# Performance work log

Measured on AMD Instinct MI355X. Metric: run time of the kernel, lower is better.

## Reference

```python
import jax, jax.numpy as jnp
import numpy as np

DIM = 256
HEADS = 8
DIM_HEAD = 32
INNER = HEADS * DIM_HEAD  # 256
SCALE = DIM_HEAD ** -0.5


def setup_inputs() -> dict:
    key = jax.random.key(0)
    k1, k2, k3, k4, k5, k6 = jax.random.split(key, 6)
    b, n, m = 2, 8192, 32
    x = jax.random.normal(k1, (b, n, DIM), dtype=jnp.float32)
    y = jax.random.normal(k2, (b, n, m, DIM), dtype=jnp.float32)
    # torch nn.Linear weights: [out, in]; store as [in, out] for x @ W
    s = 1.0 / np.sqrt(DIM)
    Wq = jax.random.uniform(k3, (DIM, INNER), jnp.float32, -s, s)
    Wkv = jax.random.uniform(k4, (DIM, 2 * INNER), jnp.float32, -s, s)
    so = 1.0 / np.sqrt(INNER)
    Wout = jax.random.uniform(k5, (INNER, DIM), jnp.float32, -so, so)
    bout = jax.random.uniform(k6, (DIM,), jnp.float32, -so, so)
    return {"x": x, "y": y, "Wq": Wq, "Wkv": Wkv, "Wout": Wout, "bout": bout}


def reference(x, y, Wq, Wkv, Wout, bout):
    b, n, m, _ = y.shape
    q = (x @ Wq).reshape(b, n, HEADS, DIM_HEAD)              # [b,n,h,d]
    kv = y @ Wkv                                              # [b,n,m,2*inner]
    k, v = jnp.split(kv, 2, axis=-1)
    k = k.reshape(b, n, m, HEADS, DIM_HEAD)                   # [b,n,m,h,d]
    v = v.reshape(b, n, m, HEADS, DIM_HEAD)
    dots = jnp.einsum('bnhd,bnmhd->bnhm', q, k) * SCALE       # per-token q_len=1 attention
    attn = jax.nn.softmax(dots, axis=-1)
    out = jnp.einsum('bnhm,bnmhd->bnhd', attn, v)
    out = out.reshape(b, n, INNER)
    return out @ Wout + bout
```

## Files before the change

kernel.cpp:

```cpp
#include <hip/hip_runtime.h>
#include <hip/hip_bf16.h>
#include <stdint.h>


typedef unsigned short u16;
typedef __attribute__((ext_vector_type(8))) short bf16x8;
typedef __attribute__((ext_vector_type(4))) float f32x4;
typedef __attribute__((ext_vector_type(4))) unsigned int u32x4;

#define NTOK 16384
#define SCALE_F 0.17677669529663687f

__device__ __forceinline__ u16 f2b(float v) {
  union { __hip_bfloat16 b; u16 s; } u;
  u.b = __float2bfloat16(v);
  return u.s;
}

__device__ __forceinline__ bf16x8 cvt8(f32x4 a, f32x4 b) {
  union { bf16x8 v; __hip_bfloat162 h[4]; } u;
  u.h[0] = __float22bfloat162_rn(float2{a[0], a[1]});
  u.h[1] = __float22bfloat162_rn(float2{a[2], a[3]});
  u.h[2] = __float22bfloat162_rn(float2{b[0], b[1]});
  u.h[3] = __float22bfloat162_rn(float2{b[2], b[3]});
  return u.v;
}

__device__ __forceinline__ void gll16(const float* g, const float* l) {
  __builtin_amdgcn_global_load_lds((const __attribute__((address_space(1))) void*)g,
                                   (__attribute__((address_space(3))) void*)l,
                                   16, 0, 0);
}

__global__ __launch_bounds__(256) void k0a(const float* __restrict__ Wq,
                                           const float* __restrict__ Wkv,
                                           u16* __restrict__ WqkT) {
  __shared__ float wq[16][260];
  __shared__ float wk[16][260];
  int tid = threadIdx.x;
  int e0 = blockIdx.x * 16, c0 = blockIdx.y * 16;
  {
    int r = tid >> 4, cs = (tid & 15) * 16;
#pragma unroll
    for (int i = 0; i < 4; i++) {
      *(f32x4*)&wq[r][cs + i * 4] = *(const f32x4*)(Wq + (e0 + r) * 256 + cs + i * 4);
      *(f32x4*)&wk[r][cs + i * 4] = *(const f32x4*)(Wkv + (c0 + r) * 512 + cs + i * 4);
    }
  }
  __syncthreads();
  int e = tid & 15, c = tid >> 4;
#pragma unroll
  for (int h = 0; h < 8; h++) {
    float acc = 0.f;
#pragma unroll
    for (int d = 0; d < 32; d++) acc += wq[e][h * 32 + d] * wk[c][h * 32 + d];
    WqkT[(h * 256 + c0 + c) * 256 + e0 + e] = f2b(acc * SCALE_F);
  }
}

__global__ __launch_bounds__(256) void k0b(const float* __restrict__ Wkv,
                                           const float* __restrict__ Wout,
                                           u16* __restrict__ WvoT) {
  __shared__ float wv[16][260];
  __shared__ float wo[256][20];
  int tid = threadIdx.x;
  int o0 = blockIdx.x * 16, c0 = blockIdx.y * 16;
  {
    int r = tid >> 4, cs = (tid & 15) * 16;
#pragma unroll
    for (int i = 0; i < 4; i++)
      *(f32x4*)&wv[r][cs + i * 4] = *(const f32x4*)(Wkv + (c0 + r) * 512 + 256 + cs + i * 4);
#pragma unroll
    for (int i = 0; i < 4; i++)
      *(f32x4*)&wo[tid][i * 4] = *(const f32x4*)(Wout + tid * 256 + o0 + i * 4);
  }
  __syncthreads();
  int o = tid >> 4, c = tid & 15;
  union { u16 s[8]; u32x4 v; } pk;
#pragma unroll
  for (int h = 0; h < 8; h++) {
    float acc = 0.f;
#pragma unroll
    for (int d = 0; d < 32; d++) acc += wv[c][h * 32 + d] * wo[h * 32 + d][o];
    pk.s[h] = f2b(acc);
  }
  *(u32x4*)(WvoT + (o0 + o) * 2048 + (c0 + c) * 8) = pk.v;
}

__global__ __launch_bounds__(256) void k1(const float* __restrict__ X,
                                          const u16* __restrict__ WqkT,
                                          u16* __restrict__ qW) {
  __shared__ u16 As[128][72];
  __shared__ u16 Bs[128][72];
  int tid = threadIdx.x;
  int wave = tid >> 6, lane = tid & 63;
  int l15 = lane & 15, kg = lane >> 4;
  int m0 = blockIdx.x * 128, n0 = blockIdx.y * 128;
  int sr = tid >> 1, sk = (tid & 1) * 32;
  f32x4 acc[4][4] = {};
  for (int kc = 0; kc < 256; kc += 64) {
#pragma unroll
    for (int i = 0; i < 4; i++) {
      f32x4 a = *(const f32x4*)(X + (size_t)(m0 + sr) * 256 + kc + sk + i * 8);
      f32x4 b = *(const f32x4*)(X + (size_t)(m0 + sr) * 256 + kc + sk + i * 8 + 4);
      *(bf16x8*)&As[sr][sk + i * 8] = cvt8(a, b);
      *(u32x4*)&Bs[sr][sk + i * 8] = *(const u32x4*)(WqkT + (n0 + sr) * 256 + kc + sk + i * 8);
    }
    __syncthreads();
    int rb = (wave >> 1) * 64, cb = (wave & 1) * 64;
#pragma unroll
    for (int ks = 0; ks < 2; ks++) {
      bf16x8 af[4], bfm[4];
#pragma unroll
      for (int i = 0; i < 4; i++) af[i] = *(const bf16x8*)&As[rb + i * 16 + l15][ks * 32 + kg * 8];
#pragma unroll
      for (int i = 0; i < 4; i++) bfm[i] = *(const bf16x8*)&Bs[cb + i * 16 + l15][ks * 32 + kg * 8];
#pragma unroll
      for (int mt = 0; mt < 4; mt++)
#pragma unroll
        for (int nt = 0; nt < 4; nt++)
          acc[mt][nt] = __builtin_amdgcn_mfma_f32_16x16x32_bf16(af[mt], bfm[nt], acc[mt][nt], 0, 0, 0);
    }
    __syncthreads();
  }
  int rb = m0 + (wave >> 1) * 64, cb = n0 + (wave & 1) * 64;
  int q = lane >> 4;
#pragma unroll
  for (int mt = 0; mt < 4; mt++)
#pragma unroll
    for (int nt = 0; nt < 4; nt++)
#pragma unroll
      for (int r = 0; r < 4; r++)
        qW[(size_t)(rb + mt * 16 + q * 4 + r) * 2048 + cb + nt * 16 + l15] = f2b(acc[mt][nt][r]);
}

__global__ __launch_bounds__(256) void k2(const float* __restrict__ Y,
                                          const u16* __restrict__ qW,
                                          u16* __restrict__ ybar) {
  __shared__ float ybuf[2][32][256];
  int tid = threadIdx.x;
  int wave = tid >> 6, lane = tid & 63;
  int l15 = lane & 15, kg = lane >> 4;
  int h8 = l15 & 7;
  int t0 = blockIdx.x * 32;

  {
    const float* g = Y + (size_t)t0 * 8192;
#pragma unroll
    for (int r = 0; r < 8; r++) {
      int row = wave * 8 + r;
      gll16(g + row * 256 + ((lane ^ (row & 7)) << 2), &ybuf[0][row][0]);
    }
  }
  __syncthreads();

#pragma unroll 1
  for (int i = 0; i < 32; i++) {
    int t = t0 + i;
    if (i + 1 < 32) {
      const float* g = Y + (size_t)(t + 1) * 8192;
      int b = (i + 1) & 1;
#pragma unroll
      for (int r = 0; r < 8; r++) {
        int row = wave * 8 + r;
        gll16(g + row * 256 + ((lane ^ (row & 7)) << 2), &ybuf[b][row][0]);
      }
    }
    const float (*buf)[256] = ybuf[i & 1];

    f32x4 D[2] = {f32x4{0.f, 0.f, 0.f, 0.f}, f32x4{0.f, 0.f, 0.f, 0.f}};
    const u16* qwt = qW + ((size_t)t << 11) + h8 * 256 + kg * 8;
    bf16x8 bfr[8];
#pragma unroll
    for (int s = 0; s < 8; s++) bfr[s] = *(const bf16x8*)(qwt + s * 32);
#pragma unroll
    for (int s = 0; s < 8; s++) {
#pragma unroll
      for (int mt = 0; mt < 2; mt++) {
        int row = mt * 16 + l15;
        int g0 = s * 8 + kg * 2;
        f32x4 y0 = *(const f32x4*)&buf[row][((g0) ^ (row & 7)) << 2];
        f32x4 y1 = *(const f32x4*)&buf[row][((g0 + 1) ^ (row & 7)) << 2];
        D[mt] = __builtin_amdgcn_mfma_f32_16x16x32_bf16(cvt8(y0, y1), bfr[s], D[mt], 0, 0, 0);
      }
    }

    float mx = -1e30f;
#pragma unroll
    for (int mt = 0; mt < 2; mt++)
#pragma unroll
      for (int r = 0; r < 4; r++) mx = fmaxf(mx, D[mt][r]);
    mx = fmaxf(mx, __shfl_xor(mx, 16));
    mx = fmaxf(mx, __shfl_xor(mx, 32));
    float sum = 0.f;
    float at[2][4];
#pragma unroll
    for (int mt = 0; mt < 2; mt++)
#pragma unroll
      for (int r = 0; r < 4; r++) {
        float e = __expf(D[mt][r] - mx);
        at[mt][r] = e;
        sum += e;
      }
    sum += __shfl_xor(sum, 16);
    sum += __shfl_xor(sum, 32);
    float inv = 1.0f / sum;
#pragma unroll
    for (int mt = 0; mt < 2; mt++)
#pragma unroll
      for (int r = 0; r < 4; r++) at[mt][r] *= inv;

    float acc0[4] = {0.f, 0.f, 0.f, 0.f};
    float acc1[4] = {0.f, 0.f, 0.f, 0.f};
#pragma unroll
    for (int mi = 0; mi < 8; mi++) {
      int mt = mi >> 2, q = mi & 3;
      float a0[4], a1[4];
#pragma unroll
      for (int r = 0; r < 4; r++) {
        a0[r] = __shfl(at[mt][r], q * 16 + wave * 2);
        a1[r] = __shfl(at[mt][r], q * 16 + wave * 2 + 1);
      }
#pragma unroll
      for (int r = 0; r < 4; r++) {
        int m = mt * 16 + q * 4 + r;
        f32x4 yv = *(const f32x4*)&buf[m][(lane ^ (m & 7)) << 2];
        acc0[0] += a0[r] * yv[0];
        acc0[1] += a0[r] * yv[1];
        acc0[2] += a0[r] * yv[2];
        acc0[3] += a0[r] * yv[3];
        acc1[0] += a1[r] * yv[0];
        acc1[1] += a1[r] * yv[1];
        acc1[2] += a1[r] * yv[2];
        acc1[3] += a1[r] * yv[3];
      }
    }
    u16* op = ybar + ((size_t)t << 11) + lane * 32 + wave * 2;
#pragma unroll
    for (int ci = 0; ci < 4; ci++) {
      __hip_bfloat162 pr = __float22bfloat162_rn(float2{acc0[ci], acc1[ci]});
      *(__hip_bfloat162*)(op + ci * 8) = pr;
    }
    __syncthreads();
  }
}

__global__ __launch_bounds__(256) void k3(const u16* __restrict__ Yb,
                                          const u16* __restrict__ WvoT,
                                          const float* __restrict__ bout,
                                          float* __restrict__ Out) {
  __shared__ u16 As[128][72];
  __shared__ u16 Bs[128][72];
  int tid = threadIdx.x;
  int wave = tid >> 6, lane = tid & 63;
  int l15 = lane & 15, kg = lane >> 4;
  int m0 = blockIdx.x * 128, n0 = blockIdx.y * 128;
  int sr = tid >> 1, sk = (tid & 1) * 32;
  f32x4 acc[4][4] = {};
#pragma unroll 1
  for (int kc = 0; kc < 2048; kc += 64) {
#pragma unroll
    for (int i = 0; i < 4; i++) {
      *(u32x4*)&As[sr][sk + i * 8] = *(const u32x4*)(Yb + (size_t)(m0 + sr) * 2048 + kc + sk + i * 8);
      *(u32x4*)&Bs[sr][sk + i * 8] = *(const u32x4*)(WvoT + (size_t)(n0 + sr) * 2048 + kc + sk + i * 8);
    }
    __syncthreads();
    int rb = (wave >> 1) * 64, cb = (wave & 1) * 64;
#pragma unroll
    for (int ks = 0; ks < 2; ks++) {
      bf16x8 af[4], bfm[4];
#pragma unroll
      for (int i = 0; i < 4; i++) af[i] = *(const bf16x8*)&As[rb + i * 16 + l15][ks * 32 + kg * 8];
#pragma unroll
      for (int i = 0; i < 4; i++) bfm[i] = *(const bf16x8*)&Bs[cb + i * 16 + l15][ks * 32 + kg * 8];
#pragma unroll
      for (int mt = 0; mt < 4; mt++)
#pragma unroll
        for (int nt = 0; nt < 4; nt++)
          acc[mt][nt] = __builtin_amdgcn_mfma_f32_16x16x32_bf16(af[mt], bfm[nt], acc[mt][nt], 0, 0, 0);
    }
    __syncthreads();
  }
  int rb = m0 + (wave >> 1) * 64, cb = n0 + (wave & 1) * 64;
  int q = lane >> 4;
#pragma unroll
  for (int nt = 0; nt < 4; nt++) {
    float bv = bout[cb + nt * 16 + l15];
#pragma unroll
    for (int mt = 0; mt < 4; mt++)
#pragma unroll
      for (int r = 0; r < 4; r++)
        Out[(size_t)(rb + mt * 16 + q * 4 + r) * 256 + cb + nt * 16 + l15] = acc[mt][nt][r] + bv;
  }
}

extern "C" void kernel_launch(void* const* d_in, const int* in_sizes, int n_in,
                              void* d_out, int out_size, void* d_ws, size_t ws_size,
                              hipStream_t stream) {
  const float* x    = (const float*)d_in[0];
  const float* y    = (const float*)d_in[1];
  const float* Wq   = (const float*)d_in[2];
  const float* Wkv  = (const float*)d_in[3];
  const float* Wout = (const float*)d_in[4];
  const float* bout = (const float*)d_in[5];
  float* out = (float*)d_out;

  char* ws = (char*)d_ws;
  u16* qW   = (u16*)(ws);
  u16* ybar = (u16*)(ws + ((size_t)64 << 20));
  u16* WqkT = (u16*)(ws + ((size_t)128 << 20));
  u16* WvoT = (u16*)(ws + ((size_t)129 << 20));

  k0a<<<dim3(16, 16), 256, 0, stream>>>(Wq, Wkv, WqkT);
  k0b<<<dim3(16, 16), 256, 0, stream>>>(Wkv, Wout, WvoT);
  k1<<<dim3(128, 16), 256, 0, stream>>>(x, WqkT, qW);
  k2<<<dim3(512), 256, 0, stream>>>(y, qW, ybar);
  k3<<<dim3(128, 2), 256, 0, stream>>>(ybar, WvoT, bout, out);
}
```

Baseline: 858.4 us.

## Restructure attention kernel to single-wave blocks with register-prefetched qW

The y-streaming attention kernel goes from 4-wave blocks covering 32 tokens each to 1-wave blocks covering 16 tokens each, launched as 1024 blocks. Each wave now computes all 8 heads per token, with attention weights passed through shared memory instead of cross-lane shuffles. The double-buffered LDS is replaced by one buffer refilled after the compute, guarded by explicit waitcnt, and the next token's qW fragments are prefetched into registers. The aims are to drop block-wide barriers, raise occupancy and widen the output stores, at the cost of less latency hiding for the y loads, since the wave stalls on vmcnt(0) each iteration.

Result: faster. 839.6 us (-2.2%).

```diff
diff --git a/kernel.cpp b/kernel.cpp
--- a/kernel.cpp
+++ b/kernel.cpp
@@ -134,45 +134,35 @@
         qW[(size_t)(rb + mt * 16 + q * 4 + r) * 2048 + cb + nt * 16 + l15] = f2b(acc[mt][nt][r]);
 }
 
-__global__ __launch_bounds__(256) void k2(const float* __restrict__ Y,
-                                          const u16* __restrict__ qW,
-                                          u16* __restrict__ ybar) {
-  __shared__ float ybuf[2][32][256];
-  int tid = threadIdx.x;
-  int wave = tid >> 6, lane = tid & 63;
+__global__ __launch_bounds__(64) void k2(const float* __restrict__ Y,
+                                         const u16* __restrict__ qW,
+                                         u16* __restrict__ ybar) {
+  __shared__ float buf[32][256];
+  __shared__ float attn_s[32][8];
+  int lane = threadIdx.x;
   int l15 = lane & 15, kg = lane >> 4;
   int h8 = l15 & 7;
-  int t0 = blockIdx.x * 32;
+  int t0 = blockIdx.x * 16;
 
   {
     const float* g = Y + (size_t)t0 * 8192;
 #pragma unroll
-    for (int r = 0; r < 8; r++) {
-      int row = wave * 8 + r;
-      gll16(g + row * 256 + ((lane ^ (row & 7)) << 2), &ybuf[0][row][0]);
-    }
-  }
-  __syncthreads();
+    for (int r = 0; r < 32; r++)
+      gll16(g + r * 256 + ((lane ^ (r & 7)) << 2), &buf[r][0]);
+  }
+  bf16x8 bfr[8];
+  {
+    const u16* qwt = qW + ((size_t)t0 << 11) + h8 * 256 + kg * 8;
+#pragma unroll
+    for (int s = 0; s < 8; s++) bfr[s] = *(const bf16x8*)(qwt + s * 32);
+  }
 
 #pragma unroll 1
-  for (int i = 0; i < 32; i++) {
+  for (int i = 0; i < 16; i++) {
     int t = t0 + i;
-    if (i + 1 < 32) {
-      const float* g = Y + (size_t)(t + 1) * 8192;
-      int b = (i + 1) & 1;
-#pragma unroll
-      for (int r = 0; r < 8; r++) {
-        int row = wave * 8 + r;
-        gll16(g + row * 256 + ((lane ^ (row & 7)) << 2), &ybuf[b][row][0]);
-      }
-    }
-    const float (*buf)[256] = ybuf[i & 1];
+    asm volatile("s_waitcnt vmcnt(0)" ::: "memory");
 
     f32x4 D[2] = {f32x4{0.f, 0.f, 0.f, 0.f}, f32x4{0.f, 0.f, 0.f, 0.f}};
-    const u16* qwt = qW + ((size_t)t << 11) + h8 * 256 + kg * 8;
-    bf16x8 bfr[8];
-#pragma unroll
-    for (int s = 0; s < 8; s++) bfr[s] = *(const bf16x8*)(qwt + s * 32);
 #pragma unroll
     for (int s = 0; s < 8; s++) {
 #pragma unroll
@@ -183,6 +173,12 @@
         f32x4 y1 = *(const f32x4*)&buf[row][((g0 + 1) ^ (row & 7)) << 2];
         D[mt] = __builtin_amdgcn_mfma_f32_16x16x32_bf16(cvt8(y0, y1), bfr[s], D[mt], 0, 0, 0);
       }
+    }
+
+    if (i + 1 < 16) {
+      const u16* qn = qW + ((size_t)(t + 1) << 11) + h8 * 256 + kg * 8;
+#pragma unroll
+      for (int s = 0; s < 8; s++) bfr[s] = *(const bf16x8*)(qn + s * 32);
     }
 
     float mx = -1e30f;
@@ -210,38 +206,49 @@
 #pragma unroll
       for (int r = 0; r < 4; r++) at[mt][r] *= inv;
 
-    float acc0[4] = {0.f, 0.f, 0.f, 0.f};
-    float acc1[4] = {0.f, 0.f, 0.f, 0.f};
-#pragma unroll
-    for (int mi = 0; mi < 8; mi++) {
-      int mt = mi >> 2, q = mi & 3;
-      float a0[4], a1[4];
-#pragma unroll
-      for (int r = 0; r < 4; r++) {
-        a0[r] = __shfl(at[mt][r], q * 16 + wave * 2);
-        a1[r] = __shfl(at[mt][r], q * 16 + wave * 2 + 1);
+    if (l15 < 8) {
+#pragma unroll
+      for (int mt = 0; mt < 2; mt++)
+#pragma unroll
+        for (int r = 0; r < 4; r++)
+          attn_s[mt * 16 + kg * 4 + r][l15] = at[mt][r];
+    }
+
+    float acc[8][4] = {};
+#pragma unroll
+    for (int m = 0; m < 32; m++) {
+      f32x4 yv = *(const f32x4*)&buf[m][(lane ^ (m & 7)) << 2];
+      f32x4 a0 = *(const f32x4*)&attn_s[m][0];
+      f32x4 a1 = *(const f32x4*)&attn_s[m][4];
+#pragma unroll
+      for (int h = 0; h < 4; h++)
+#pragma unroll
+        for (int c = 0; c < 4; c++) {
+          acc[h][c]     += a0[h] * yv[c];
+          acc[h + 4][c] += a1[h] * yv[c];
+        }
+    }
+
+    asm volatile("s_waitcnt lgkmcnt(0)" ::: "memory");
+
+    if (i + 1 < 16) {
+      const float* g = Y + (size_t)(t + 1) * 8192;
+#pragma unroll
+      for (int r = 0; r < 32; r++)
+        gll16(g + r * 256 + ((lane ^ (r & 7)) << 2), &buf[r][0]);
+    }
+
+    u16* op = ybar + ((size_t)t << 11) + lane * 32;
+#pragma unroll
+    for (int ci = 0; ci < 4; ci++) {
+      union { u16 s[8]; u32x4 v; } pk;
+#pragma unroll
+      for (int j = 0; j < 4; j++) {
+        __hip_bfloat162 pr = __float22bfloat162_rn(float2{acc[2 * j][ci], acc[2 * j + 1][ci]});
+        *(__hip_bfloat162*)&pk.s[2 * j] = pr;
       }
-#pragma unroll
-      for (int r = 0; r < 4; r++) {
-        int m = mt * 16 + q * 4 + r;
-        f32x4 yv = *(const f32x4*)&buf[m][(lane ^ (m & 7)) << 2];
-        acc0[0] += a0[r] * yv[0];
-        acc0[1] += a0[r] * yv[1];
-        acc0[2] += a0[r] * yv[2];
-        acc0[3] += a0[r] * yv[3];
-        acc1[0] += a1[r] * yv[0];
-        acc1[1] += a1[r] * yv[1];
-        acc1[2] += a1[r] * yv[2];
-        acc1[3] += a1[r] * yv[3];
-      }
-    }
-    u16* op = ybar + ((size_t)t << 11) + lane * 32 + wave * 2;
-#pragma unroll
-    for (int ci = 0; ci < 4; ci++) {
-      __hip_bfloat162 pr = __float22bfloat162_rn(float2{acc0[ci], acc1[ci]});
-      *(__hip_bfloat162*)(op + ci * 8) = pr;
-    }
-    __syncthreads();
+      *(u32x4*)(op + ci * 8) = pk.v;
+    }
   }
 }
 
@@ -314,6 +321,6 @@
   k0a<<<dim3(16, 16), 256, 0, stream>>>(Wq, Wkv, WqkT);
   k0b<<<dim3(16, 16), 256, 0, stream>>>(Wkv, Wout, WvoT);
   k1<<<dim3(128, 16), 256, 0, stream>>>(x, WqkT, qW);
-  k2<<<dim3(512), 256, 0, stream>>>(y, qW, ybar);
+  k2<<<dim3(1024), 64, 0, stream>>>(y, qW, ybar);
   k3<<<dim3(128, 2), 256, 0, stream>>>(ybar, WvoT, bout, out);
 }
```
